# Kernel optimization log

Hardware: AMD Instinct MI355X
Metric: run time of the kernel (lower is better)

The kernel has to match this reference:

```python
import jax, jax.numpy as jnp
import numpy as np


def setup_inputs() -> dict:
    key = jax.random.key(0)
    ks = jax.random.split(key, 7)
    B, T, D, H, A = 1024, 512, 32, 128, 10
    s = lambda *sh: 1.0 / np.sqrt(H)
    return {
        "x": jax.random.normal(ks[0], (B, T, D), dtype=jnp.float32),
        "W_ih": jax.random.normal(ks[1], (4 * H, D), dtype=jnp.float32) * (1.0 / np.sqrt(H)),
        "W_hh": jax.random.normal(ks[2], (4 * H, H), dtype=jnp.float32) * (1.0 / np.sqrt(H)),
        "b_ih": jax.random.normal(ks[3], (4 * H,), dtype=jnp.float32) * (1.0 / np.sqrt(H)),
        "b_hh": jax.random.normal(ks[4], (4 * H,), dtype=jnp.float32) * (1.0 / np.sqrt(H)),
        "fc_w": jax.random.normal(ks[5], (A, H), dtype=jnp.float32) * (1.0 / np.sqrt(H)),
        "fc_b": jax.random.normal(ks[6], (A,), dtype=jnp.float32) * (1.0 / np.sqrt(H)),
    }


def _lstm(x, W_ih, W_hh, b_ih, b_hh):
    # x: (B, T, D). PyTorch gate order: i, f, g, o packed along 4H rows.
    B, T, D = x.shape
    H = W_hh.shape[1]
    # Precompute input projections for all timesteps in one GEMM: (B,T,4H)
    x_proj = jnp.einsum('btd,gd->btg', x, W_ih) + b_ih + b_hh
    h0 = jnp.zeros((B, H), dtype=x.dtype)
    c0 = jnp.zeros((B, H), dtype=x.dtype)

    def step(carry, xp_t):
        h, c = carry
        gates = xp_t + h @ W_hh.T  # (B, 4H)
        i, f, g, o = jnp.split(gates, 4, axis=-1)
        i = jax.nn.sigmoid(i)
        f = jax.nn.sigmoid(f)
        g = jnp.tanh(g)
        o = jax.nn.sigmoid(o)
        c_new = f * c + i * g
        h_new = o * jnp.tanh(c_new)
        return (h_new, c_new), None

    (h_n, c_n), _ = jax.lax.scan(step, (h0, c0), jnp.swapaxes(x_proj, 0, 1))
    return h_n, c_n


def reference(x, W_ih, W_hh, b_ih, b_hh, fc_w, fc_b):
    h_n, c_n = _lstm(x, W_ih, W_hh, b_ih, b_hh)
    # out[:, -1, :] == h_n for a single-layer LSTM
    q_values = h_n @ fc_w.T + fc_b  # (B, A)
    return q_values, h_n[None], c_n[None]  # hidden states with num_layers=1 leading dim
```

## Files before the change

kernel.cpp:

```cpp
#include <hip/hip_runtime.h>

typedef short  short8  __attribute__((ext_vector_type(8)));
typedef float  floatx4 __attribute__((ext_vector_type(4)));

#define TT 512
#define DD 32
#define HH 128
#define AA 10
#define LOG2E 1.44269504088896340736f

__device__ __forceinline__ unsigned f2bf(float f) {
    unsigned u = __builtin_bit_cast(unsigned, f);
    return (u + 0x7fffu + ((u >> 16) & 1u)) >> 16;
}

__device__ __forceinline__ short8 cvt8(floatx4 a, floatx4 b) {
    short8 r;
    r[0] = (short)f2bf(a[0]); r[1] = (short)f2bf(a[1]);
    r[2] = (short)f2bf(a[2]); r[3] = (short)f2bf(a[3]);
    r[4] = (short)f2bf(b[0]); r[5] = (short)f2bf(b[1]);
    r[6] = (short)f2bf(b[2]); r[7] = (short)f2bf(b[3]);
    return r;
}

__device__ __forceinline__ float sig2(float a) {
    return __builtin_amdgcn_rcpf(1.0f + __builtin_amdgcn_exp2f(a));
}
__device__ __forceinline__ float tanh2(float a) {
    return 1.0f - 2.0f * __builtin_amdgcn_rcpf(1.0f + __builtin_amdgcn_exp2f(a));
}

__device__ __forceinline__ void step_barrier() {
    asm volatile("s_waitcnt lgkmcnt(0)" ::: "memory");
    __builtin_amdgcn_s_barrier();
    asm volatile("" ::: "memory");
}

__global__ __launch_bounds__(256)
void xcvt(const float* __restrict__ x, unsigned short* __restrict__ xb) {
    const long i = (long)blockIdx.x * 256 + threadIdx.x;
    floatx4 a = *(const floatx4*)(x + 8 * i);
    floatx4 b = *(const floatx4*)(x + 8 * i + 4);
    *(short8*)(xb + 8 * i) = cvt8(a, b);
}

template<int USEWS>
__global__ __launch_bounds__(512, 2)
void lstm_fused(const float* __restrict__ x,    const unsigned short* __restrict__ xbf,
                const float* __restrict__ W_ih, const float* __restrict__ W_hh,
                const float* __restrict__ b_ih, const float* __restrict__ b_hh,
                const float* __restrict__ fc_w, const float* __restrict__ fc_b,
                float* __restrict__ out)
{
    __shared__ unsigned short h_lds[2][4 * HH];
    __shared__ float hq[4][HH + 4];

    const int tid  = threadIdx.x;
    const int lane = tid & 63;
    const int w    = tid >> 6;
    const int l15  = lane & 15;
    const int lgrp = lane >> 4;
    const int bloc = l15 & 3;

    const long bglob = (long)blockIdx.x * 4 + bloc;

    short8  afr[4][5];
    floatx4 biasv[4];
    #pragma unroll
    for (int tg = 0; tg < 4; ++tg) {
        const float sc = (tg == 2) ? (2.0f * LOG2E) : (-LOG2E);
        const int m  = w + 8 * tg;
        const int ga = 16 * m + l15;
        #pragma unroll
        for (int s = 0; s < 4; ++s) {
            const float* p = W_hh + ga * HH + 32 * s + 8 * lgrp;
            afr[tg][s] = cvt8(*(const floatx4*)p * sc, *(const floatx4*)(p + 4) * sc);
        }
        {
            const float* p = W_ih + ga * DD + 8 * lgrp;
            afr[tg][4] = cvt8(*(const floatx4*)p * sc, *(const floatx4*)(p + 4) * sc);
        }
        #pragma unroll
        for (int r = 0; r < 4; ++r) {
            const int gd = 16 * m + 4 * lgrp + r;
            biasv[tg][r] = (b_ih[gd] + b_hh[gd]) * sc;
        }
    }

    ((unsigned*)h_lds)[tid] = 0u;
    __syncthreads();

    const int rs  = l15 >> 2;
    const bool sb0 = (rs & 1) != 0;
    const bool sb1 = (rs & 2) != 0;
    const int bp  = bloc;
    const int jp  = 16 * w + 4 * lgrp + rs;

    int rdA0, rdA1, rdA2, rdA3, rdB0, rdB1, rdB2, rdB3;
    {
        const int rb = bloc * 256;
        rdA0 = rb + ((64 * 0 + 16 * lgrp + 32 * bloc) & 255);
        rdA1 = rb + ((64 * 1 + 16 * lgrp + 32 * bloc) & 255);
        rdA2 = rb + ((64 * 2 + 16 * lgrp + 32 * bloc) & 255);
        rdA3 = rb + ((64 * 3 + 16 * lgrp + 32 * bloc) & 255);
        rdB0 = rdA0 + 1024; rdB1 = rdA1 + 1024; rdB2 = rdA2 + 1024; rdB3 = rdA3 + 1024;
    }
    const int wrA = bp * 256 + ((2 * jp + 32 * bp) & 255);
    const int wrB = wrA + 1024;

    short8  xf;
    floatx4 xa, xb_;
    if constexpr (USEWS) {
        xf = *(const short8*)(xbf + (bglob * TT) * DD + 8 * lgrp);
    } else {
        xa  = *(const floatx4*)(x + (bglob * TT) * DD + 8 * lgrp);
        xb_ = *(const floatx4*)(x + (bglob * TT) * DD + 8 * lgrp + 4);
    }

    float cval = 0.f, hval = 0.f;
    const char* lbase = (const char*)h_lds;

    auto STEP = [&](int r0, int r1, int r2, int r3, int wro, int t) {
        short8 xcur;
        const int tn = (t + 1 < TT) ? (t + 1) : (TT - 1);
        if constexpr (USEWS) {
            xcur = xf;
            xf = *(const short8*)(xbf + (bglob * TT + tn) * DD + 8 * lgrp);
        } else {
            xcur = cvt8(xa, xb_);
            const float* xp = x + (bglob * TT + tn) * DD + 8 * lgrp;
            xa  = *(const floatx4*)(xp);
            xb_ = *(const floatx4*)(xp + 4);
        }

        short8 hb0 = *(const short8*)(lbase + r0);
        short8 hb1 = *(const short8*)(lbase + r1);
        short8 hb2 = *(const short8*)(lbase + r2);
        short8 hb3 = *(const short8*)(lbase + r3);

        floatx4 acc[4];
        #pragma unroll
        for (int tg = 0; tg < 4; ++tg)
            acc[tg] = __builtin_amdgcn_mfma_f32_16x16x32_bf16(afr[tg][4], xcur, biasv[tg], 0, 0, 0);
        #pragma unroll
        for (int tg = 0; tg < 4; ++tg)
            acc[tg] = __builtin_amdgcn_mfma_f32_16x16x32_bf16(afr[tg][0], hb0, acc[tg], 0, 0, 0);
        #pragma unroll
        for (int tg = 0; tg < 4; ++tg)
            acc[tg] = __builtin_amdgcn_mfma_f32_16x16x32_bf16(afr[tg][1], hb1, acc[tg], 0, 0, 0);
        #pragma unroll
        for (int tg = 0; tg < 4; ++tg)
            acc[tg] = __builtin_amdgcn_mfma_f32_16x16x32_bf16(afr[tg][2], hb2, acc[tg], 0, 0, 0);
        #pragma unroll
        for (int tg = 0; tg < 4; ++tg)
            acc[tg] = __builtin_amdgcn_mfma_f32_16x16x32_bf16(afr[tg][3], hb3, acc[tg], 0, 0, 0);

        float g4[4];
        #pragma unroll
        for (int tg = 0; tg < 4; ++tg) {
            const float v01 = sb0 ? acc[tg][1] : acc[tg][0];
            const float v23 = sb0 ? acc[tg][3] : acc[tg][2];
            g4[tg] = sb1 ? v23 : v01;
        }

        const float iv = sig2(g4[0]);
        const float fv = sig2(g4[1]);
        const float gv = tanh2(g4[2]);
        const float ov = sig2(g4[3]);
        cval = fv * cval + iv * gv;
        hval = ov * tanh2(cval * (2.0f * LOG2E));

        *(unsigned short*)((char*)h_lds + wro) = (unsigned short)f2bf(hval);
        step_barrier();
    };

    #pragma unroll 1
    for (int t = 0; t < TT; t += 2) {
        STEP(rdA0, rdA1, rdA2, rdA3, wrB, t);
        STEP(rdB0, rdB1, rdB2, rdB3, wrA, t + 1);
    }

    {
        const long bg = (long)blockIdx.x * 4 + bp;
        out[10240 + bg * HH + jp]          = hval;
        out[10240 + 131072 + bg * HH + jp] = cval;
        hq[bp][jp] = hval;
    }
    __syncthreads();
    if (tid < 4 * AA) {
        const int b = tid / AA, a = tid - AA * b;
        float s = fc_b[a];
        const float* fw = fc_w + a * HH;
        const float* hr = &hq[b][0];
        #pragma unroll 8
        for (int j = 0; j < HH; ++j) s = fmaf(hr[j], fw[j], s);
        out[((long)blockIdx.x * 4 + b) * AA + a] = s;
    }
}

extern "C" void kernel_launch(void* const* d_in, const int* in_sizes, int n_in,
                              void* d_out, int out_size, void* d_ws, size_t ws_size,
                              hipStream_t stream) {
    const float* x    = (const float*)d_in[0];
    const float* W_ih = (const float*)d_in[1];
    const float* W_hh = (const float*)d_in[2];
    const float* b_ih = (const float*)d_in[3];
    const float* b_hh = (const float*)d_in[4];
    const float* fc_w = (const float*)d_in[5];
    const float* fc_b = (const float*)d_in[6];
    float* out = (float*)d_out;

    const size_t xelems = (size_t)1024 * TT * DD;
    if (ws_size >= xelems * sizeof(unsigned short)) {
        unsigned short* xb = (unsigned short*)d_ws;
        xcvt<<<dim3(8192), dim3(256), 0, stream>>>(x, xb);
        lstm_fused<1><<<dim3(256), dim3(512), 0, stream>>>(
            x, xb, W_ih, W_hh, b_ih, b_hh, fc_w, fc_b, out);
    } else {
        lstm_fused<0><<<dim3(256), dim3(512), 0, stream>>>(
            x, nullptr, W_ih, W_hh, b_ih, b_hh, fc_w, fc_b, out);
    }
}
```

Measured before the change: 299.6 us.

## Halve LSTM block to 4 waves, each computing two hidden-unit tiles

New measurement: 360.4 us. +20.3%, slower.

```diff
diff --git a/kernel.cpp b/kernel.cpp
--- a/kernel.cpp
+++ b/kernel.cpp
@@ -45,7 +45,7 @@
 }
 
 template<int USEWS>
-__global__ __launch_bounds__(512, 2)
+__global__ __launch_bounds__(256, 1)
 void lstm_fused(const float* __restrict__ x,    const unsigned short* __restrict__ xbf,
                 const float* __restrict__ W_ih, const float* __restrict__ W_hh,
                 const float* __restrict__ b_ih, const float* __restrict__ b_hh,
@@ -64,49 +64,51 @@
 
     const long bglob = (long)blockIdx.x * 4 + bloc;
 
-    short8  afr[4][5];
-    floatx4 biasv[4];
+    short8  afr[4][2][5];
+    floatx4 biasv[4][2];
     #pragma unroll
     for (int tg = 0; tg < 4; ++tg) {
         const float sc = (tg == 2) ? (2.0f * LOG2E) : (-LOG2E);
-        const int m  = w + 8 * tg;
-        const int ga = 16 * m + l15;
-        #pragma unroll
-        for (int s = 0; s < 4; ++s) {
-            const float* p = W_hh + ga * HH + 32 * s + 8 * lgrp;
-            afr[tg][s] = cvt8(*(const floatx4*)p * sc, *(const floatx4*)(p + 4) * sc);
+        #pragma unroll
+        for (int jb = 0; jb < 2; ++jb) {
+            const int ga = 128 * tg + 16 * (2 * w + jb) + l15;
+            #pragma unroll
+            for (int s = 0; s < 4; ++s) {
+                const float* p = W_hh + ga * HH + 32 * s + 8 * lgrp;
+                afr[tg][jb][s] = cvt8(*(const floatx4*)p * sc, *(const floatx4*)(p + 4) * sc);
+            }
+            {
+                const float* p = W_ih + ga * DD + 8 * lgrp;
+                afr[tg][jb][4] = cvt8(*(const floatx4*)p * sc, *(const floatx4*)(p + 4) * sc);
+            }
+            #pragma unroll
+            for (int r = 0; r < 4; ++r) {
+                const int gd = 128 * tg + 16 * (2 * w + jb) + 4 * lgrp + r;
+                biasv[tg][jb][r] = (b_ih[gd] + b_hh[gd]) * sc;
+            }
         }
-        {
-            const float* p = W_ih + ga * DD + 8 * lgrp;
-            afr[tg][4] = cvt8(*(const floatx4*)p * sc, *(const floatx4*)(p + 4) * sc);
-        }
-        #pragma unroll
-        for (int r = 0; r < 4; ++r) {
-            const int gd = 16 * m + 4 * lgrp + r;
-            biasv[tg][r] = (b_ih[gd] + b_hh[gd]) * sc;
-        }
-    }
-
-    ((unsigned*)h_lds)[tid] = 0u;
+    }
+
+    ((unsigned*)h_lds)[tid]       = 0u;
+    ((unsigned*)h_lds)[tid + 256] = 0u;
     __syncthreads();
 
     const int rs  = l15 >> 2;
     const bool sb0 = (rs & 1) != 0;
     const bool sb1 = (rs & 2) != 0;
     const int bp  = bloc;
-    const int jp  = 16 * w + 4 * lgrp + rs;
-
-    int rdA0, rdA1, rdA2, rdA3, rdB0, rdB1, rdB2, rdB3;
-    {
-        const int rb = bloc * 256;
-        rdA0 = rb + ((64 * 0 + 16 * lgrp + 32 * bloc) & 255);
-        rdA1 = rb + ((64 * 1 + 16 * lgrp + 32 * bloc) & 255);
-        rdA2 = rb + ((64 * 2 + 16 * lgrp + 32 * bloc) & 255);
-        rdA3 = rb + ((64 * 3 + 16 * lgrp + 32 * bloc) & 255);
-        rdB0 = rdA0 + 1024; rdB1 = rdA1 + 1024; rdB2 = rdA2 + 1024; rdB3 = rdA3 + 1024;
-    }
-    const int wrA = bp * 256 + ((2 * jp + 32 * bp) & 255);
-    const int wrB = wrA + 1024;
+    const int jp0 = 32 * w + 4 * lgrp + rs;
+    const int jp1 = jp0 + 16;
+
+    const int rb = bloc * 256;
+    const int rdA0 = rb + ((16 * lgrp + 32 * bloc) & 255);
+    const int rdA1 = rb + ((64 + 16 * lgrp + 32 * bloc) & 255);
+    const int rdA2 = rb + ((128 + 16 * lgrp + 32 * bloc) & 255);
+    const int rdA3 = rb + ((192 + 16 * lgrp + 32 * bloc) & 255);
+    const int rdB0 = rdA0 + 1024, rdB1 = rdA1 + 1024, rdB2 = rdA2 + 1024, rdB3 = rdA3 + 1024;
+    const int wrA0 = bp * 256 + ((2 * jp0 + 32 * bp) & 255);
+    const int wrA1 = bp * 256 + ((2 * jp1 + 32 * bp) & 255);
+    const int wrB0 = wrA0 + 1024, wrB1 = wrA1 + 1024;
 
     short8  xf;
     floatx4 xa, xb_;
@@ -117,10 +119,10 @@
         xb_ = *(const floatx4*)(x + (bglob * TT) * DD + 8 * lgrp + 4);
     }
 
-    float cval = 0.f, hval = 0.f;
+    float cv0 = 0.f, cv1 = 0.f, hv0 = 0.f, hv1 = 0.f;
     const char* lbase = (const char*)h_lds;
 
-    auto STEP = [&](int r0, int r1, int r2, int r3, int wro, int t) {
+    auto STEP = [&](int r0, int r1, int r2, int r3, int wo0, int wo1, int t) {
         short8 xcur;
         const int tn = (t + 1 < TT) ? (t + 1) : (TT - 1);
         if constexpr (USEWS) {
@@ -138,53 +140,74 @@
         short8 hb2 = *(const short8*)(lbase + r2);
         short8 hb3 = *(const short8*)(lbase + r3);
 
-        floatx4 acc[4];
-        #pragma unroll
-        for (int tg = 0; tg < 4; ++tg)
-            acc[tg] = __builtin_amdgcn_mfma_f32_16x16x32_bf16(afr[tg][4], xcur, biasv[tg], 0, 0, 0);
-        #pragma unroll
-        for (int tg = 0; tg < 4; ++tg)
-            acc[tg] = __builtin_amdgcn_mfma_f32_16x16x32_bf16(afr[tg][0], hb0, acc[tg], 0, 0, 0);
-        #pragma unroll
-        for (int tg = 0; tg < 4; ++tg)
-            acc[tg] = __builtin_amdgcn_mfma_f32_16x16x32_bf16(afr[tg][1], hb1, acc[tg], 0, 0, 0);
-        #pragma unroll
-        for (int tg = 0; tg < 4; ++tg)
-            acc[tg] = __builtin_amdgcn_mfma_f32_16x16x32_bf16(afr[tg][2], hb2, acc[tg], 0, 0, 0);
-        #pragma unroll
-        for (int tg = 0; tg < 4; ++tg)
-            acc[tg] = __builtin_amdgcn_mfma_f32_16x16x32_bf16(afr[tg][3], hb3, acc[tg], 0, 0, 0);
-
-        float g4[4];
+        floatx4 acc[4][2];
+        #pragma unroll
+        for (int tg = 0; tg < 4; ++tg)
+            #pragma unroll
+            for (int jb = 0; jb < 2; ++jb)
+                acc[tg][jb] = __builtin_amdgcn_mfma_f32_16x16x32_bf16(afr[tg][jb][4], xcur, biasv[tg][jb], 0, 0, 0);
+        #pragma unroll
+        for (int tg = 0; tg < 4; ++tg)
+            #pragma unroll
+            for (int jb = 0; jb < 2; ++jb)
+                acc[tg][jb] = __builtin_amdgcn_mfma_f32_16x16x32_bf16(afr[tg][jb][0], hb0, acc[tg][jb], 0, 0, 0);
+        #pragma unroll
+        for (int tg = 0; tg < 4; ++tg)
+            #pragma unroll
+            for (int jb = 0; jb < 2; ++jb)
+                acc[tg][jb] = __builtin_amdgcn_mfma_f32_16x16x32_bf16(afr[tg][jb][1], hb1, acc[tg][jb], 0, 0, 0);
+        #pragma unroll
+        for (int tg = 0; tg < 4; ++tg)
+            #pragma unroll
+            for (int jb = 0; jb < 2; ++jb)
+                acc[tg][jb] = __builtin_amdgcn_mfma_f32_16x16x32_bf16(afr[tg][jb][2], hb2, acc[tg][jb], 0, 0, 0);
+        #pragma unroll
+        for (int tg = 0; tg < 4; ++tg)
+            #pragma unroll
+            for (int jb = 0; jb < 2; ++jb)
+                acc[tg][jb] = __builtin_amdgcn_mfma_f32_16x16x32_bf16(afr[tg][jb][3], hb3, acc[tg][jb], 0, 0, 0);
+
+        float g0[4], g1[4];
         #pragma unroll
         for (int tg = 0; tg < 4; ++tg) {
-            const float v01 = sb0 ? acc[tg][1] : acc[tg][0];
-            const float v23 = sb0 ? acc[tg][3] : acc[tg][2];
-            g4[tg] = sb1 ? v23 : v01;
+            const float a01 = sb0 ? acc[tg][0][1] : acc[tg][0][0];
+            const float a23 = sb0 ? acc[tg][0][3] : acc[tg][0][2];
+            g0[tg] = sb1 ? a23 : a01;
+            const float b01 = sb0 ? acc[tg][1][1] : acc[tg][1][0];
+            const float b23 = sb0 ? acc[tg][1][3] : acc[tg][1][2];
+            g1[tg] = sb1 ? b23 : b01;
         }
 
-        const float iv = sig2(g4[0]);
-        const float fv = sig2(g4[1]);
-        const float gv = tanh2(g4[2]);
-        const float ov = sig2(g4[3]);
-        cval = fv * cval + iv * gv;
-        hval = ov * tanh2(cval * (2.0f * LOG2E));
-
-        *(unsigned short*)((char*)h_lds + wro) = (unsigned short)f2bf(hval);
+        const float iv0 = sig2(g0[0]), iv1 = sig2(g1[0]);
+        const float fv0 = sig2(g0[1]), fv1 = sig2(g1[1]);
+        const float gv0 = tanh2(g0[2]), gv1 = tanh2(g1[2]);
+        const float ov0 = sig2(g0[3]), ov1 = sig2(g1[3]);
+        cv0 = fv0 * cv0 + iv0 * gv0;
+        cv1 = fv1 * cv1 + iv1 * gv1;
+        hv0 = ov0 * tanh2(cv0 * (2.0f * LOG2E));
+        hv1 = ov1 * tanh2(cv1 * (2.0f * LOG2E));
+
+        unsigned hp;
+        asm("v_cvt_pk_bf16_f32 %0, %1, %2" : "=v"(hp) : "v"(hv0), "v"(hv1));
+        *(unsigned short*)((char*)h_lds + wo0) = (unsigned short)hp;
+        *(unsigned short*)((char*)h_lds + wo1) = (unsigned short)(hp >> 16);
         step_barrier();
     };
 
     #pragma unroll 1
     for (int t = 0; t < TT; t += 2) {
-        STEP(rdA0, rdA1, rdA2, rdA3, wrB, t);
-        STEP(rdB0, rdB1, rdB2, rdB3, wrA, t + 1);
+        STEP(rdA0, rdA1, rdA2, rdA3, wrB0, wrB1, t);
+        STEP(rdB0, rdB1, rdB2, rdB3, wrA0, wrA1, t + 1);
     }
 
     {
         const long bg = (long)blockIdx.x * 4 + bp;
-        out[10240 + bg * HH + jp]          = hval;
-        out[10240 + 131072 + bg * HH + jp] = cval;
-        hq[bp][jp] = hval;
+        out[10240 + bg * HH + jp0]          = hv0;
+        out[10240 + bg * HH + jp1]          = hv1;
+        out[10240 + 131072 + bg * HH + jp0] = cv0;
+        out[10240 + 131072 + bg * HH + jp1] = cv1;
+        hq[bp][jp0] = hv0;
+        hq[bp][jp1] = hv1;
     }
     __syncthreads();
     if (tid < 4 * AA) {
@@ -214,10 +237,10 @@
     if (ws_size >= xelems * sizeof(unsigned short)) {
         unsigned short* xb = (unsigned short*)d_ws;
         xcvt<<<dim3(8192), dim3(256), 0, stream>>>(x, xb);
-        lstm_fused<1><<<dim3(256), dim3(512), 0, stream>>>(
+        lstm_fused<1><<<dim3(256), dim3(256), 0, stream>>>(
             x, xb, W_ih, W_hh, b_ih, b_hh, fc_w, fc_b, out);
     } else {
-        lstm_fused<0><<<dim3(256), dim3(512), 0, stream>>>(
+        lstm_fused<0><<<dim3(256), dim3(256), 0, stream>>>(
             x, nullptr, W_ih, W_hh, b_ih, b_hh, fc_w, fc_b, out);
     }
 }
```

## Repartition LSTM blocks to two batch rows with 4 waves and doubled MFMA tiles

Applied to the files above, without the earlier changes.

New measurement: 531.3 us. +77.3%, slower.

```diff
diff --git a/kernel.cpp b/kernel.cpp
--- a/kernel.cpp
+++ b/kernel.cpp
@@ -45,68 +45,68 @@
 }
 
 template<int USEWS>
-__global__ __launch_bounds__(512, 2)
+__global__ __launch_bounds__(256, 2)
 void lstm_fused(const float* __restrict__ x,    const unsigned short* __restrict__ xbf,
                 const float* __restrict__ W_ih, const float* __restrict__ W_hh,
                 const float* __restrict__ b_ih, const float* __restrict__ b_hh,
                 const float* __restrict__ fc_w, const float* __restrict__ fc_b,
                 float* __restrict__ out)
 {
-    __shared__ unsigned short h_lds[2][4 * HH];
-    __shared__ float hq[4][HH + 4];
+    __shared__ unsigned short h_lds[2][2 * HH];
+    __shared__ float hq[2][HH + 4];
 
     const int tid  = threadIdx.x;
     const int lane = tid & 63;
     const int w    = tid >> 6;
     const int l15  = lane & 15;
     const int lgrp = lane >> 4;
-    const int bloc = l15 & 3;
-
-    const long bglob = (long)blockIdx.x * 4 + bloc;
-
-    short8  afr[4][5];
-    floatx4 biasv[4];
+    const int bloc = l15 & 1;
+
+    const long bglob = (long)blockIdx.x * 2 + bloc;
+
+    short8  afr[4][2][5];
+    floatx4 biasv[4][2];
     #pragma unroll
     for (int tg = 0; tg < 4; ++tg) {
         const float sc = (tg == 2) ? (2.0f * LOG2E) : (-LOG2E);
-        const int m  = w + 8 * tg;
-        const int ga = 16 * m + l15;
-        #pragma unroll
-        for (int s = 0; s < 4; ++s) {
-            const float* p = W_hh + ga * HH + 32 * s + 8 * lgrp;
-            afr[tg][s] = cvt8(*(const floatx4*)p * sc, *(const floatx4*)(p + 4) * sc);
-        }
-        {
-            const float* p = W_ih + ga * DD + 8 * lgrp;
-            afr[tg][4] = cvt8(*(const floatx4*)p * sc, *(const floatx4*)(p + 4) * sc);
-        }
-        #pragma unroll
-        for (int r = 0; r < 4; ++r) {
-            const int gd = 16 * m + 4 * lgrp + r;
-            biasv[tg][r] = (b_ih[gd] + b_hh[gd]) * sc;
+        #pragma unroll
+        for (int jb = 0; jb < 2; ++jb) {
+            const int ga = 128 * tg + 32 * w + 16 * jb + l15;
+            #pragma unroll
+            for (int s = 0; s < 4; ++s) {
+                const float* p = W_hh + ga * HH + 32 * s + 8 * lgrp;
+                afr[tg][jb][s] = cvt8(*(const floatx4*)p * sc, *(const floatx4*)(p + 4) * sc);
+            }
+            {
+                const float* p = W_ih + ga * DD + 8 * lgrp;
+                afr[tg][jb][4] = cvt8(*(const floatx4*)p * sc, *(const floatx4*)(p + 4) * sc);
+            }
+            #pragma unroll
+            for (int r = 0; r < 4; ++r) {
+                const int gd = 128 * tg + 32 * w + 16 * jb + 4 * lgrp + r;
+                biasv[tg][jb][r] = (b_ih[gd] + b_hh[gd]) * sc;
+            }
         }
     }
 
     ((unsigned*)h_lds)[tid] = 0u;
     __syncthreads();
 
-    const int rs  = l15 >> 2;
-    const bool sb0 = (rs & 1) != 0;
-    const bool sb1 = (rs & 2) != 0;
+    const int jbL = (l15 >> 3) & 1;
+    const int rL  = (l15 >> 1) & 3;
+    const bool sr0 = (rL & 1) != 0;
+    const bool sr1 = (rL & 2) != 0;
+    const bool sjb = jbL != 0;
     const int bp  = bloc;
-    const int jp  = 16 * w + 4 * lgrp + rs;
-
-    int rdA0, rdA1, rdA2, rdA3, rdB0, rdB1, rdB2, rdB3;
-    {
-        const int rb = bloc * 256;
-        rdA0 = rb + ((64 * 0 + 16 * lgrp + 32 * bloc) & 255);
-        rdA1 = rb + ((64 * 1 + 16 * lgrp + 32 * bloc) & 255);
-        rdA2 = rb + ((64 * 2 + 16 * lgrp + 32 * bloc) & 255);
-        rdA3 = rb + ((64 * 3 + 16 * lgrp + 32 * bloc) & 255);
-        rdB0 = rdA0 + 1024; rdB1 = rdA1 + 1024; rdB2 = rdA2 + 1024; rdB3 = rdA3 + 1024;
-    }
-    const int wrA = bp * 256 + ((2 * jp + 32 * bp) & 255);
-    const int wrB = wrA + 1024;
+    const int jp  = 32 * w + 16 * jbL + 4 * lgrp + rL;
+
+    const int rdA0 = bloc * 256 + ((       16 * lgrp + 64 * bloc) & 255);
+    const int rdA1 = bloc * 256 + (( 64 +  16 * lgrp + 64 * bloc) & 255);
+    const int rdA2 = bloc * 256 + ((128 +  16 * lgrp + 64 * bloc) & 255);
+    const int rdA3 = bloc * 256 + ((192 +  16 * lgrp + 64 * bloc) & 255);
+    const int rdB0 = rdA0 + 512, rdB1 = rdA1 + 512, rdB2 = rdA2 + 512, rdB3 = rdA3 + 512;
+    const int wrA  = bp * 256 + ((2 * jp + 64 * bp) & 255);
+    const int wrB  = wrA + 512;
 
     short8  xf;
     floatx4 xa, xb_;
@@ -138,29 +138,45 @@
         short8 hb2 = *(const short8*)(lbase + r2);
         short8 hb3 = *(const short8*)(lbase + r3);
 
-        floatx4 acc[4];
-        #pragma unroll
-        for (int tg = 0; tg < 4; ++tg)
-            acc[tg] = __builtin_amdgcn_mfma_f32_16x16x32_bf16(afr[tg][4], xcur, biasv[tg], 0, 0, 0);
-        #pragma unroll
-        for (int tg = 0; tg < 4; ++tg)
-            acc[tg] = __builtin_amdgcn_mfma_f32_16x16x32_bf16(afr[tg][0], hb0, acc[tg], 0, 0, 0);
-        #pragma unroll
-        for (int tg = 0; tg < 4; ++tg)
-            acc[tg] = __builtin_amdgcn_mfma_f32_16x16x32_bf16(afr[tg][1], hb1, acc[tg], 0, 0, 0);
-        #pragma unroll
-        for (int tg = 0; tg < 4; ++tg)
-            acc[tg] = __builtin_amdgcn_mfma_f32_16x16x32_bf16(afr[tg][2], hb2, acc[tg], 0, 0, 0);
-        #pragma unroll
-        for (int tg = 0; tg < 4; ++tg)
-            acc[tg] = __builtin_amdgcn_mfma_f32_16x16x32_bf16(afr[tg][3], hb3, acc[tg], 0, 0, 0);
+        floatx4 acc[4][2];
+        __builtin_amdgcn_s_setprio(1);
+        #pragma unroll
+        for (int tg = 0; tg < 4; ++tg)
+            #pragma unroll
+            for (int jb = 0; jb < 2; ++jb)
+                acc[tg][jb] = __builtin_amdgcn_mfma_f32_16x16x32_bf16(afr[tg][jb][4], xcur, biasv[tg][jb], 0, 0, 0);
+        #pragma unroll
+        for (int tg = 0; tg < 4; ++tg)
+            #pragma unroll
+            for (int jb = 0; jb < 2; ++jb)
+                acc[tg][jb] = __builtin_amdgcn_mfma_f32_16x16x32_bf16(afr[tg][jb][0], hb0, acc[tg][jb], 0, 0, 0);
+        #pragma unroll
+        for (int tg = 0; tg < 4; ++tg)
+            #pragma unroll
+            for (int jb = 0; jb < 2; ++jb)
+                acc[tg][jb] = __builtin_amdgcn_mfma_f32_16x16x32_bf16(afr[tg][jb][1], hb1, acc[tg][jb], 0, 0, 0);
+        #pragma unroll
+        for (int tg = 0; tg < 4; ++tg)
+            #pragma unroll
+            for (int jb = 0; jb < 2; ++jb)
+                acc[tg][jb] = __builtin_amdgcn_mfma_f32_16x16x32_bf16(afr[tg][jb][2], hb2, acc[tg][jb], 0, 0, 0);
+        #pragma unroll
+        for (int tg = 0; tg < 4; ++tg)
+            #pragma unroll
+            for (int jb = 0; jb < 2; ++jb)
+                acc[tg][jb] = __builtin_amdgcn_mfma_f32_16x16x32_bf16(afr[tg][jb][3], hb3, acc[tg][jb], 0, 0, 0);
+        __builtin_amdgcn_s_setprio(0);
 
         float g4[4];
         #pragma unroll
         for (int tg = 0; tg < 4; ++tg) {
-            const float v01 = sb0 ? acc[tg][1] : acc[tg][0];
-            const float v23 = sb0 ? acc[tg][3] : acc[tg][2];
-            g4[tg] = sb1 ? v23 : v01;
+            const float a01 = sr0 ? acc[tg][0][1] : acc[tg][0][0];
+            const float a23 = sr0 ? acc[tg][0][3] : acc[tg][0][2];
+            const float va  = sr1 ? a23 : a01;
+            const float b01 = sr0 ? acc[tg][1][1] : acc[tg][1][0];
+            const float b23 = sr0 ? acc[tg][1][3] : acc[tg][1][2];
+            const float vb  = sr1 ? b23 : b01;
+            g4[tg] = sjb ? vb : va;
         }
 
         const float iv = sig2(g4[0]);
@@ -181,20 +197,20 @@
     }
 
     {
-        const long bg = (long)blockIdx.x * 4 + bp;
+        const long bg = (long)blockIdx.x * 2 + bp;
         out[10240 + bg * HH + jp]          = hval;
         out[10240 + 131072 + bg * HH + jp] = cval;
         hq[bp][jp] = hval;
     }
     __syncthreads();
-    if (tid < 4 * AA) {
+    if (tid < 2 * AA) {
         const int b = tid / AA, a = tid - AA * b;
         float s = fc_b[a];
         const float* fw = fc_w + a * HH;
         const float* hr = &hq[b][0];
         #pragma unroll 8
         for (int j = 0; j < HH; ++j) s = fmaf(hr[j], fw[j], s);
-        out[((long)blockIdx.x * 4 + b) * AA + a] = s;
+        out[((long)blockIdx.x * 2 + b) * AA + a] = s;
     }
 }
 
@@ -214,10 +230,10 @@
     if (ws_size >= xelems * sizeof(unsigned short)) {
         unsigned short* xb = (unsigned short*)d_ws;
         xcvt<<<dim3(8192), dim3(256), 0, stream>>>(x, xb);
-        lstm_fused<1><<<dim3(256), dim3(512), 0, stream>>>(
+        lstm_fused<1><<<dim3(512), dim3(256), 0, stream>>>(
             x, xb, W_ih, W_hh, b_ih, b_hh, fc_w, fc_b, out);
     } else {
-        lstm_fused<0><<<dim3(256), dim3(512), 0, stream>>>(
+        lstm_fused<0><<<dim3(512), dim3(256), 0, stream>>>(
             x, nullptr, W_ih, W_hh, b_ih, b_hh, fc_w, fc_b, out);
     }
 }
```
